# Kernel tuning notes

Hardware: AMD Instinct MI355X
Metric: run time of the kernel (lower is better)

The kernel has to match this reference:

```python
import jax, jax.numpy as jnp
import numpy as np
from jax import lax

# --- RPN config (eval / TEST path) ---
ASPECT = (0.5, 1.0, 2.0)
SCALE = (8.0, 16.0, 32.0)
STRIDE = 16
N_ANCHORS = len(ASPECT) * len(SCALE)  # 9
PRE_NMS = 6000
POST_NMS = 300
NMS_THRESH = 0.7
MIN_SIZE = 16.0
NEG = jnp.float32(-1e9)


def conv2d(x, w, b, pad):
    y = lax.conv_general_dilated(x, w, (1, 1), [(pad, pad), (pad, pad)],
                                 dimension_numbers=('NCHW', 'OIHW', 'NCHW'))
    return y + b[None, :, None, None]


def make_anchors(h, w):
    asp = jnp.array(ASPECT, jnp.float32)
    sc = jnp.array(SCALE, jnp.float32)
    size = float(STRIDE * STRIDE)
    ws = (jnp.sqrt(size / asp)[:, None] * sc[None, :]).reshape(-1)  # (A,)
    hs = (jnp.sqrt(size * asp)[:, None] * sc[None, :]).reshape(-1)
    c = (STRIDE - 1) / 2.0
    base = jnp.stack([c - 0.5 * (ws - 1), c - 0.5 * (hs - 1),
                      c + 0.5 * (ws - 1), c + 0.5 * (hs - 1)], axis=-1)  # (A,4)
    sx = jnp.arange(w, dtype=jnp.float32) * STRIDE
    sy = jnp.arange(h, dtype=jnp.float32) * STRIDE
    shift_x, shift_y = jnp.meshgrid(sx, sy)  # (h,w)
    shifts = jnp.stack([shift_x, shift_y, shift_x, shift_y], axis=-1)  # (h,w,4)
    return (shifts[:, :, None, :] + base[None, None]).reshape(-1, 4)  # (h*w*A,4)


def decode_boxes(anchors, deltas):
    wa = anchors[..., 2] - anchors[..., 0] + 1.0
    ha = anchors[..., 3] - anchors[..., 1] + 1.0
    cxa = anchors[..., 0] + 0.5 * wa
    cya = anchors[..., 1] + 0.5 * ha
    cx = deltas[..., 0] * wa + cxa
    cy = deltas[..., 1] * ha + cya
    pw = jnp.exp(deltas[..., 2]) * wa
    ph = jnp.exp(deltas[..., 3]) * ha
    return jnp.stack([cx - 0.5 * pw, cy - 0.5 * ph,
                      cx + 0.5 * pw, cy + 0.5 * ph], axis=-1)


def iou_one_many(box, boxes):
    x1 = jnp.maximum(box[0], boxes[:, 0])
    y1 = jnp.maximum(box[1], boxes[:, 1])
    x2 = jnp.minimum(box[2], boxes[:, 2])
    y2 = jnp.minimum(box[3], boxes[:, 3])
    inter = jnp.maximum(0.0, x2 - x1 + 1.0) * jnp.maximum(0.0, y2 - y1 + 1.0)
    a0 = (box[2] - box[0] + 1.0) * (box[3] - box[1] + 1.0)
    a1 = (boxes[:, 2] - boxes[:, 0] + 1.0) * (boxes[:, 3] - boxes[:, 1] + 1.0)
    return inter / (a0 + a1 - inter)


def nms_keep(boxes, scores):
    # boxes: (PRE,4) sorted by score desc; returns POST_NMS kept indices
    n = boxes.shape[0]

    def body(i, carry):
        valid, keep = carry
        s = jnp.where(valid, scores, NEG)
        j = jnp.argmax(s).astype(jnp.int32)
        keep = keep.at[i].set(j)
        iou = iou_one_many(boxes[j], boxes)
        valid = valid & (iou <= NMS_THRESH)
        valid = valid.at[j].set(False)
        return valid, keep

    _, keep = lax.fori_loop(0, POST_NMS, body,
                            (jnp.ones(n, bool), jnp.zeros(POST_NMS, jnp.int32)))
    return keep


def rpn_forward(input, im_info, w_feat, b_feat, w_cls, b_cls, w_reg, b_reg):
    feat = jax.nn.relu(conv2d(input, w_feat, b_feat, 1))  # (B,512,h,w)
    cls = conv2d(feat, w_cls, b_cls, 0)                    # (B,2A,h,w)
    B, _, h, w = cls.shape
    prob = jax.nn.softmax(cls.reshape(B, N_ANCHORS, 2, h, w), axis=2)
    fg = prob[:, :, 1]                                     # (B,A,h,w)
    scores = fg.transpose(0, 2, 3, 1).reshape(B, h * w * N_ANCHORS)
    reg = conv2d(feat, w_reg, b_reg, 0)                    # (B,4A,h,w)
    deltas = reg.transpose(0, 2, 3, 1).reshape(B, h * w * N_ANCHORS, 4)

    anchors = make_anchors(h, w)                           # (K,4)
    boxes = decode_boxes(anchors[None], deltas)            # (B,K,4)

    # clip to image
    im_h = im_info[:, 0][:, None]
    im_w = im_info[:, 1][:, None]
    x1 = jnp.clip(boxes[..., 0], 0.0, im_w - 1.0)
    y1 = jnp.clip(boxes[..., 1], 0.0, im_h - 1.0)
    x2 = jnp.clip(boxes[..., 2], 0.0, im_w - 1.0)
    y2 = jnp.clip(boxes[..., 3], 0.0, im_h - 1.0)
    boxes = jnp.stack([x1, y1, x2, y2], axis=-1)

    # min-size filter (mask scores instead of dropping rows)
    ms = MIN_SIZE * im_info[:, 2][:, None]
    ok = ((x2 - x1 + 1.0) >= ms) & ((y2 - y1 + 1.0) >= ms)
    scores = jnp.where(ok, scores, NEG)

    top_scores, order = lax.top_k(scores, PRE_NMS)         # (B,PRE)
    boxes_sorted = jnp.take_along_axis(boxes, order[..., None], axis=1)
    keep = jax.vmap(nms_keep)(boxes_sorted, top_scores)    # (B,POST)
    rois_boxes = jnp.take_along_axis(boxes_sorted, keep[..., None], axis=1)
    bidx = jnp.broadcast_to(jnp.arange(B, dtype=boxes.dtype)[:, None, None],
                            (B, POST_NMS, 1))
    return jnp.concatenate([bidx, rois_boxes], axis=-1)    # (B,POST,5)


def setup_inputs() -> dict:
    key = jax.random.key(0)
    ks = jax.random.split(key, 8)
    B, C, H, W = 8, 512, 64, 64
    inp = {
        'input': jax.random.normal(ks[0], (B, C, H, W), jnp.float32),
        'gt_box': jnp.zeros((B, 20, 5), jnp.float32),
        'im_info': jnp.tile(jnp.array([[1024.0, 1024.0, 1.0]], jnp.float32), (B, 1)),
        'w_feat': jax.random.normal(ks[1], (512, 512, 3, 3), jnp.float32) * 0.01,
        'b_feat': jnp.zeros((512,), jnp.float32),
        'w_cls': jax.random.normal(ks[2], (2 * N_ANCHORS, 512, 1, 1), jnp.float32) * 0.01,
        'b_cls': jnp.zeros((2 * N_ANCHORS,), jnp.float32),
        'w_reg': jax.random.normal(ks[3], (4 * N_ANCHORS, 512, 1, 1), jnp.float32) * 0.01,
        'b_reg': jnp.zeros((4 * N_ANCHORS,), jnp.float32),
    }
    return inp


def reference(input, gt_box, im_info, w_feat, b_feat, w_cls, b_cls, w_reg, b_reg):
    # eval-mode RPN: module returns (0, 0, rois); we return rois
    return rpn_forward(input, im_info, w_feat, b_feat, w_cls, b_cls, w_reg, b_reg)
```

## Files before the change

### kernel.cpp

```cpp
#include <hip/hip_runtime.h>
#include <hip/hip_bf16.h>
#include <stdint.h>

#define HW      64
#define CIN     512
#define KOUT    512
#define BATCH   8
#define NANCH   9
#define NBOX    (HW*HW*NANCH)
#define PRE_NMS 6000
#define POST_NMS 300
#define SORT_N  8192

__global__ __launch_bounds__(256, 2)
void conv3x3_relu(const float* __restrict__ in, const float* __restrict__ w,
                  const float* __restrict__ bias, float* __restrict__ feat) {
    __shared__ float s_in[2][8][6][68];
    __shared__ float s_w3[2][72 * 72];

    const int tid = threadIdx.x;
    const int k0  = blockIdx.x * 64;
    const int y0  = blockIdx.y * 4;
    const int b   = blockIdx.z;
    const int kg  = tid & 7;
    const int pos = tid >> 3;
    const int tx  = pos & 15;
    const int ty  = pos >> 4;
    const int x0  = tx * 4;

    int in_lds[3]; int in_goff[3]; bool in_ok[3];
#pragma unroll
    for (int s = 0; s < 3; ++s) {
        int v  = tid + 256 * s;
        int ci = v / 96, rem = v % 96;
        int r  = rem >> 4, c4 = rem & 15;
        int gy = y0 - 1 + r;
        in_ok[s]  = ((unsigned)gy < 64u);
        int gyc   = gy < 0 ? 0 : (gy > 63 ? 63 : gy);
        in_lds[s] = (ci * 6 + r) * 68 + 1 + 4 * c4;
        in_goff[s] = ((b * 512 + ci) * 64 + gyc) * 64 + 4 * c4;
    }
    int w_lds[5]; int w_goff[5]; bool w_ok[5];
#pragma unroll
    for (int s = 0; s < 5; ++s) {
        int q = tid + 256 * s;
        w_ok[s] = (q < 1152);
        int qq = w_ok[s] ? q : 0;
        int k = qq / 18, j4 = qq % 18;
        w_lds[s]  = (j4 * 4) * 72 + k;
        w_goff[s] = (k0 + k) * 4608 + 4 * j4;
    }

    for (int i = tid; i < 2 * 8 * 6 * 68; i += 256) ((float*)s_in)[i] = 0.0f;

    float4 pin[3], pw[5];
    auto prefetch = [&](int ch) {
#pragma unroll
        for (int s = 0; s < 3; ++s)
            pin[s] = *(const float4*)&in[in_goff[s] + ch * 4096];
#pragma unroll
        for (int s = 0; s < 5; ++s)
            pw[s] = *(const float4*)&w[w_goff[s] + ch * 9];
    };
    prefetch(0);

    float acc[2][8][4];
#pragma unroll
    for (int r = 0; r < 2; ++r)
#pragma unroll
        for (int k = 0; k < 8; ++k)
#pragma unroll
            for (int c = 0; c < 4; ++c) acc[r][k][c] = 0.0f;

    for (int cc8 = 0; cc8 < 64; ++cc8) {
        float* SIN = &s_in[cc8 & 1][0][0][0];
        float* SW  = &s_w3[cc8 & 1][0];

#pragma unroll
        for (int s = 0; s < 3; ++s) if (in_ok[s]) {
            SIN[in_lds[s] + 0] = pin[s].x;
            SIN[in_lds[s] + 1] = pin[s].y;
            SIN[in_lds[s] + 2] = pin[s].z;
            SIN[in_lds[s] + 3] = pin[s].w;
        }
#pragma unroll
        for (int s = 0; s < 5; ++s) if (w_ok[s]) {
            SW[w_lds[s] + 0 * 72] = pw[s].x;
            SW[w_lds[s] + 1 * 72] = pw[s].y;
            SW[w_lds[s] + 2 * 72] = pw[s].z;
            SW[w_lds[s] + 3 * 72] = pw[s].w;
        }
        __syncthreads();
        if (cc8 < 63) prefetch((cc8 + 1) * 8);

#pragma unroll
        for (int ci = 0; ci < 8; ++ci) {
#pragma unroll
            for (int dy = 0; dy < 3; ++dy) {
                float iv[2][6];
#pragma unroll
                for (int rr = 0; rr < 2; ++rr) {
                    int r = ty * 2 + rr + dy;
                    const float* rowp = &SIN[(ci * 6 + r) * 68];
                    float4 va = *(const float4*)&rowp[x0];
                    float2 vb = *(const float2*)&rowp[x0 + 4];
                    iv[rr][0] = va.x; iv[rr][1] = va.y; iv[rr][2] = va.z;
                    iv[rr][3] = va.w; iv[rr][4] = vb.x; iv[rr][5] = vb.y;
                }
#pragma unroll
                for (int dx = 0; dx < 3; ++dx) {
                    const float* wp = &SW[(ci * 9 + dy * 3 + dx) * 72 + kg * 8];
                    float4 w0v = *(const float4*)wp;
                    float4 w1v = *(const float4*)(wp + 4);
                    float wv[8] = {w0v.x, w0v.y, w0v.z, w0v.w,
                                   w1v.x, w1v.y, w1v.z, w1v.w};
#pragma unroll
                    for (int rr = 0; rr < 2; ++rr)
#pragma unroll
                        for (int k = 0; k < 8; ++k)
#pragma unroll
                            for (int c = 0; c < 4; ++c)
                                acc[rr][k][c] = fmaf(iv[rr][dx + c], wv[k], acc[rr][k][c]);
                }
            }
        }
    }
#pragma unroll
    for (int k = 0; k < 8; ++k) {
        float bv = bias[k0 + kg * 8 + k];
#pragma unroll
        for (int rr = 0; rr < 2; ++rr) {
            int y = y0 + ty * 2 + rr;
            float4 o;
            o.x = fmaxf(acc[rr][k][0] + bv, 0.0f);
            o.y = fmaxf(acc[rr][k][1] + bv, 0.0f);
            o.z = fmaxf(acc[rr][k][2] + bv, 0.0f);
            o.w = fmaxf(acc[rr][k][3] + bv, 0.0f);
            *(float4*)&feat[(((size_t)b * KOUT + k0 + kg * 8 + k) * HW + y) * HW + x0] = o;
        }
    }
}

__global__ __launch_bounds__(256, 2)
void heads(const float* __restrict__ feat,
           const float* __restrict__ wcls, const float* __restrict__ bcls,
           const float* __restrict__ wreg, const float* __restrict__ breg,
           const float* __restrict__ iminfo,
           unsigned long long* __restrict__ keys, float4* __restrict__ pbox) {
    __shared__ float s_w[128 * 56];

    const int tid = threadIdx.x;
    const int pix = blockIdx.x * 256 + tid;
    const int b   = pix >> 12;
    const int rem = pix & 4095;
    const int y   = rem >> 6;
    const int x   = rem & 63;

    float acc[54];
#pragma unroll
    for (int j = 0; j < 54; ++j) acc[j] = 0.0f;

    for (int cc = 0; cc < 512; cc += 128) {
        __syncthreads();
        for (int i = tid; i < 128 * 54; i += 256) {
            int j = i / 128; int cl = i % 128;
            float v = (j < 18) ? wcls[(size_t)j * 512 + cc + cl]
                               : wreg[(size_t)(j - 18) * 512 + cc + cl];
            s_w[cl * 56 + j] = v;
        }
        __syncthreads();
#pragma unroll 8
        for (int c2 = 0; c2 < 128; ++c2) {
            float f = feat[(((size_t)b * 512 + cc + c2) * 64 + y) * 64 + x];
#pragma unroll
            for (int j = 0; j < 54; ++j)
                acc[j] = fmaf(f, s_w[c2 * 56 + j], acc[j]);
        }
    }

    const float im_h = iminfo[b * 3 + 0];
    const float im_w = iminfo[b * 3 + 1];
    const float ms   = 16.0f * iminfo[b * 3 + 2];
    const float ASP[3] = {0.5f, 1.0f, 2.0f};
    const float SCL[3] = {8.0f, 16.0f, 32.0f};

#pragma unroll
    for (int a = 0; a < 9; ++a) {
        float c0 = acc[2 * a]     + bcls[2 * a];
        float c1 = acc[2 * a + 1] + bcls[2 * a + 1];
        float m  = fmaxf(c0, c1);
        float e0 = expf(c0 - m), e1 = expf(c1 - m);
        float fg = e1 / (e0 + e1);

        float d0 = acc[18 + 4 * a + 0] + breg[4 * a + 0];
        float d1 = acc[18 + 4 * a + 1] + breg[4 * a + 1];
        float d2 = acc[18 + 4 * a + 2] + breg[4 * a + 2];
        float d3 = acc[18 + 4 * a + 3] + breg[4 * a + 3];

        int ai = a / 3, si = a % 3;
        float wsz = sqrtf(256.0f / ASP[ai]) * SCL[si];
        float hsz = sqrtf(256.0f * ASP[ai]) * SCL[si];
        float sx = (float)x * 16.0f, sy = (float)y * 16.0f;
        float x1a = sx + (7.5f - 0.5f * (wsz - 1.0f));
        float y1a = sy + (7.5f - 0.5f * (hsz - 1.0f));
        float x2a = sx + (7.5f + 0.5f * (wsz - 1.0f));
        float y2a = sy + (7.5f + 0.5f * (hsz - 1.0f));

        float wa = x2a - x1a + 1.0f, ha = y2a - y1a + 1.0f;
        float cxa = x1a + 0.5f * wa, cya = y1a + 0.5f * ha;
        float cx = d0 * wa + cxa, cy = d1 * ha + cya;
        float pw = expf(d2) * wa, ph = expf(d3) * ha;
        float bx1 = cx - 0.5f * pw, by1 = cy - 0.5f * ph;
        float bx2 = cx + 0.5f * pw, by2 = cy + 0.5f * ph;

        bx1 = fminf(fmaxf(bx1, 0.0f), im_w - 1.0f);
        by1 = fminf(fmaxf(by1, 0.0f), im_h - 1.0f);
        bx2 = fminf(fmaxf(bx2, 0.0f), im_w - 1.0f);
        by2 = fminf(fmaxf(by2, 0.0f), im_h - 1.0f);

        bool ok = (bx2 - bx1 + 1.0f >= ms) && (by2 - by1 + 1.0f >= ms);
        float s = ok ? fg : -1e9f;

        unsigned u = __float_as_uint(s);
        u = (u & 0x80000000u) ? ~u : (u | 0x80000000u);
        int idx = (y * 64 + x) * 9 + a;
        keys[(size_t)b * NBOX + idx] =
            ((unsigned long long)u << 32) | (unsigned)(~(unsigned)idx);
        pbox[(size_t)b * NBOX + idx] = make_float4(bx1, by1, bx2, by2);
    }
}

__global__ __launch_bounds__(1024)
void select_sort(const unsigned long long* __restrict__ keys,
                 const float4* __restrict__ pbox,
                 float4* __restrict__ sorted) {
    __shared__ unsigned long long sbuf[SORT_N];
    __shared__ unsigned hist[16][256];
    __shared__ unsigned sh_prefix, sh_remaining, sh_counter;

    const int tid = threadIdx.x;
    const int b   = blockIdx.x;
    const int wv  = tid >> 6;
    const unsigned long long* kb = keys + (size_t)b * NBOX;

    if (tid == 0) { sh_prefix = 0u; sh_remaining = PRE_NMS; sh_counter = 0u; }

    for (int p = 3; p >= 0; --p) {
        for (int i = tid; i < 16 * 256; i += 1024) ((unsigned*)hist)[i] = 0u;
        __syncthreads();
        unsigned prefix = sh_prefix;
        unsigned pmask  = (p == 3) ? 0u : (0xFFFFFFFFu << (8 * (p + 1)));
        for (int i = tid; i < NBOX; i += 1024) {
            unsigned u = (unsigned)(kb[i] >> 32);
            if ((u & pmask) == prefix)
                atomicAdd(&hist[wv][(u >> (8 * p)) & 255], 1u);
        }
        __syncthreads();
        if (tid < 256) {
            unsigned s = 0;
#pragma unroll
            for (int w2 = 0; w2 < 16; ++w2) s += hist[w2][tid];
            hist[0][tid] = s;
        }
        __syncthreads();
        if (tid == 0) {
            unsigned rem = sh_remaining;
            int v = 255;
            for (; v > 0; --v) {
                unsigned c = hist[0][v];
                if (rem <= c) break;
                rem -= c;
            }
            sh_prefix    = prefix | ((unsigned)v << (8 * p));
            sh_remaining = rem;
        }
        __syncthreads();
    }
    const unsigned thr = sh_prefix;

    for (int i = tid; i < NBOX; i += 1024) {
        unsigned long long k = kb[i];
        bool act = ((unsigned)(k >> 32) >= thr);
        unsigned long long bal = __ballot(act);
        if (act) {
            int lane   = tid & 63;
            int leader = __ffsll(bal) - 1;
            unsigned base = 0;
            if (lane == leader) base = atomicAdd(&sh_counter, (unsigned)__popcll(bal));
            base = __shfl(base, leader);
            unsigned off = (unsigned)__popcll(bal & ((1ull << lane) - 1ull));
            unsigned pos2 = base + off;
            if (pos2 < SORT_N) sbuf[pos2] = k;
        }
    }
    __syncthreads();
    unsigned n = sh_counter; if (n > SORT_N) n = SORT_N;
    for (int i = (int)n + tid; i < SORT_N; i += 1024) sbuf[i] = 0ull;
    __syncthreads();

    for (int k = 2; k <= SORT_N; k <<= 1) {
        for (int j = k >> 1; j > 0; j >>= 1) {
            for (int t = tid; t < SORT_N / 2; t += 1024) {
                int i  = ((t & ~(j - 1)) << 1) | (t & (j - 1));
                int ix = i | j;
                bool up = ((i & k) == 0);
                unsigned long long a = sbuf[i], c = sbuf[ix];
                bool sw = up ? (a < c) : (a > c);
                if (sw) { sbuf[i] = c; sbuf[ix] = a; }
            }
            __syncthreads();
        }
    }

    for (int i = tid; i < PRE_NMS; i += 1024) {
        unsigned idx = ~((unsigned)sbuf[i]);
        sorted[(size_t)b * PRE_NMS + i] = pbox[(size_t)b * NBOX + idx];
    }
}

__global__ __launch_bounds__(512, 2)
void nms(const float4* __restrict__ sorted, float* __restrict__ out) {
    __shared__ unsigned long long vmask[94];
    __shared__ int sh_j;

    const int tid = threadIdx.x;
    const int b   = blockIdx.x;
    const float4* sb = sorted + (size_t)b * PRE_NMS;

    float4 bx[12]; float ar[12];
#pragma unroll
    for (int s = 0; s < 12; ++s) {
        int i = tid + 512 * s;
        if (i < PRE_NMS) {
            float4 v = sb[i];
            bx[s] = v;
            ar[s] = (v.z - v.x + 1.0f) * (v.w - v.y + 1.0f);
        } else {
            bx[s] = make_float4(0.f, 0.f, 0.f, 0.f);
            ar[s] = 1.0f;
        }
    }
    if (tid < 94) vmask[tid] = (tid < 93) ? ~0ull : ((1ull << 48) - 1ull);
    __syncthreads();

    for (int it = 0; it < POST_NMS; ++it) {
        if (tid < 64) {
            unsigned long long w0 = vmask[tid];
            unsigned long long w1 = (tid < 30) ? vmask[tid + 64] : 0ull;
            int cand = w0 ? (tid * 64 + __ffsll(w0) - 1)
                          : (w1 ? ((tid + 64) * 64 + __ffsll(w1) - 1) : 0x7FFFFFFF);
#pragma unroll
            for (int off = 32; off > 0; off >>= 1) {
                int o = __shfl_xor(cand, off);
                cand = (o < cand) ? o : cand;
            }
            if (tid == 0) sh_j = (cand == 0x7FFFFFFF) ? 0 : cand;
        }
        __syncthreads();
        int j = sh_j;
        float4 jb = sb[j];
        if (tid == 0) {
            float* o = out + ((size_t)b * POST_NMS + it) * 5;
            o[0] = (float)b; o[1] = jb.x; o[2] = jb.y; o[3] = jb.z; o[4] = jb.w;
        }
        float ja = (jb.z - jb.x + 1.0f) * (jb.w - jb.y + 1.0f);
#pragma unroll
        for (int s = 0; s < 12; ++s) {
            int i = tid + 512 * s;
            if (i < PRE_NMS && ((vmask[i >> 6] >> (i & 63)) & 1ull)) {
                float xx1 = fmaxf(jb.x, bx[s].x);
                float yy1 = fmaxf(jb.y, bx[s].y);
                float xx2 = fminf(jb.z, bx[s].z);
                float yy2 = fminf(jb.w, bx[s].w);
                float inter = fmaxf(0.0f, xx2 - xx1 + 1.0f) *
                              fmaxf(0.0f, yy2 - yy1 + 1.0f);
                float iou = inter / (ja + ar[s] - inter);
                if (iou > 0.7f)
                    atomicAnd(&vmask[i >> 6], ~(1ull << (i & 63)));
            }
        }
        __syncthreads();
    }
}

extern "C" void kernel_launch(void* const* d_in, const int* in_sizes, int n_in,
                              void* d_out, int out_size, void* d_ws, size_t ws_size,
                              hipStream_t stream) {
    (void)in_sizes; (void)n_in; (void)out_size; (void)ws_size;
    const float* input  = (const float*)d_in[0];
    const float* iminfo = (const float*)d_in[2];
    const float* wfeat  = (const float*)d_in[3];
    const float* bfeat  = (const float*)d_in[4];
    const float* wcls   = (const float*)d_in[5];
    const float* bcls   = (const float*)d_in[6];
    const float* wreg   = (const float*)d_in[7];
    const float* breg   = (const float*)d_in[8];
    float* out = (float*)d_out;

    char* ws = (char*)d_ws;
    float*               feat   = (float*)ws;
    unsigned long long*  keys   = (unsigned long long*)(ws + 67108864);
    float4*              pbox   = (float4*)(ws + 67108864 + 2359296);
    float4*              sorted = (float4*)(ws + 67108864 + 2359296 + 4718592);

    conv3x3_relu<<<dim3(8, 16, 8), 256, 0, stream>>>(input, wfeat, bfeat, feat);
    heads<<<dim3(128), 256, 0, stream>>>(feat, wcls, bcls, wreg, breg, iminfo, keys, pbox);
    select_sort<<<dim3(8), 1024, 0, stream>>>(keys, pbox, sorted);
    nms<<<dim3(8), 512, 0, stream>>>(sorted, out);
}
```

Baseline: 3.177 ms.

## Pre-transpose conv weights and double conv tile height with unpadded input tiles

Adds a kernel that transposes the 3x3 conv weights to [cin*9][kout] once per call, so weight tiles load as coalesced float4 rows and store to LDS as float4 instead of scattered scalars. The conv tile grows from 4 to 8 output rows per block, giving 4 rows x 8 channels x 4 columns of accumulators per thread. This raises FMA reuse of each weight load and halves the grid. Input rows are stored unpadded and the x-halo is read per element with edge masking. The cost is higher register pressure under launch_bounds(256,2), an extra launch, and reuse of the keys workspace region for the transposed weights, which heads later overwrites.

```diff
diff --git a/kernel.cpp b/kernel.cpp
--- a/kernel.cpp
+++ b/kernel.cpp
@@ -12,15 +12,33 @@
 #define POST_NMS 300
 #define SORT_N  8192
 
+__global__ __launch_bounds__(256)
+void transpose_w(const float* __restrict__ w, float* __restrict__ wt) {
+    __shared__ float t[32][33];
+    const int jt = blockIdx.x * 32, kt = blockIdx.y * 32;
+    const int c  = threadIdx.x & 31, r8 = threadIdx.x >> 5;
+#pragma unroll
+    for (int p = 0; p < 4; ++p) {
+        int kl = r8 + p * 8;
+        t[kl][c] = w[(size_t)(kt + kl) * 4608 + jt + c];
+    }
+    __syncthreads();
+#pragma unroll
+    for (int p = 0; p < 4; ++p) {
+        int jl = r8 + p * 8;
+        wt[(size_t)(jt + jl) * 512 + kt + c] = t[c][jl];
+    }
+}
+
 __global__ __launch_bounds__(256, 2)
-void conv3x3_relu(const float* __restrict__ in, const float* __restrict__ w,
+void conv3x3_relu(const float* __restrict__ in, const float* __restrict__ wt,
                   const float* __restrict__ bias, float* __restrict__ feat) {
-    __shared__ float s_in[2][8][6][68];
-    __shared__ float s_w3[2][72 * 72];
+    __shared__ float s_in[2][8][10][64];
+    __shared__ float s_w[2][72][64];
 
     const int tid = threadIdx.x;
     const int k0  = blockIdx.x * 64;
-    const int y0  = blockIdx.y * 4;
+    const int y0  = blockIdx.y * 8;
     const int b   = blockIdx.z;
     const int kg  = tid & 7;
     const int pos = tid >> 3;
@@ -28,16 +46,16 @@
     const int ty  = pos >> 4;
     const int x0  = tx * 4;
 
-    int in_lds[3]; int in_goff[3]; bool in_ok[3];
-#pragma unroll
-    for (int s = 0; s < 3; ++s) {
-        int v  = tid + 256 * s;
-        int ci = v / 96, rem = v % 96;
+    int in_lds[5]; int in_goff[5]; bool in_ok[5];
+#pragma unroll
+    for (int s = 0; s < 5; ++s) {
+        int q  = tid + 256 * s;
+        int ci = q / 160, rem = q % 160;
         int r  = rem >> 4, c4 = rem & 15;
         int gy = y0 - 1 + r;
         in_ok[s]  = ((unsigned)gy < 64u);
         int gyc   = gy < 0 ? 0 : (gy > 63 ? 63 : gy);
-        in_lds[s] = (ci * 6 + r) * 68 + 1 + 4 * c4;
+        in_lds[s] = (ci * 10 + r) * 64 + 4 * c4;
         in_goff[s] = ((b * 512 + ci) * 64 + gyc) * 64 + 4 * c4;
     }
     int w_lds[5]; int w_goff[5]; bool w_ok[5];
@@ -46,27 +64,26 @@
         int q = tid + 256 * s;
         w_ok[s] = (q < 1152);
         int qq = w_ok[s] ? q : 0;
-        int k = qq / 18, j4 = qq % 18;
-        w_lds[s]  = (j4 * 4) * 72 + k;
-        w_goff[s] = (k0 + k) * 4608 + 4 * j4;
-    }
-
-    for (int i = tid; i < 2 * 8 * 6 * 68; i += 256) ((float*)s_in)[i] = 0.0f;
-
-    float4 pin[3], pw[5];
-    auto prefetch = [&](int ch) {
-#pragma unroll
-        for (int s = 0; s < 3; ++s)
-            pin[s] = *(const float4*)&in[in_goff[s] + ch * 4096];
+        int jl = qq / 16, k4 = qq % 16;
+        w_lds[s]  = jl * 64 + 4 * k4;
+        w_goff[s] = jl * 512 + k0 + 4 * k4;
+    }
+
+    float4 pin[5], pw[5];
+    const float4 z4 = make_float4(0.f, 0.f, 0.f, 0.f);
+    auto prefetch = [&](int cc8) {
 #pragma unroll
         for (int s = 0; s < 5; ++s)
-            pw[s] = *(const float4*)&w[w_goff[s] + ch * 9];
+            pin[s] = in_ok[s] ? *(const float4*)&in[in_goff[s] + cc8 * 32768] : z4;
+#pragma unroll
+        for (int s = 0; s < 5; ++s)
+            if (w_ok[s]) pw[s] = *(const float4*)&wt[(size_t)cc8 * 36864 + w_goff[s]];
     };
     prefetch(0);
 
-    float acc[2][8][4];
-#pragma unroll
-    for (int r = 0; r < 2; ++r)
+    float acc[4][8][4];
+#pragma unroll
+    for (int r = 0; r < 4; ++r)
 #pragma unroll
         for (int k = 0; k < 8; ++k)
 #pragma unroll
@@ -74,53 +91,49 @@
 
     for (int cc8 = 0; cc8 < 64; ++cc8) {
         float* SIN = &s_in[cc8 & 1][0][0][0];
-        float* SW  = &s_w3[cc8 & 1][0];
-
-#pragma unroll
-        for (int s = 0; s < 3; ++s) if (in_ok[s]) {
-            SIN[in_lds[s] + 0] = pin[s].x;
-            SIN[in_lds[s] + 1] = pin[s].y;
-            SIN[in_lds[s] + 2] = pin[s].z;
-            SIN[in_lds[s] + 3] = pin[s].w;
-        }
-#pragma unroll
-        for (int s = 0; s < 5; ++s) if (w_ok[s]) {
-            SW[w_lds[s] + 0 * 72] = pw[s].x;
-            SW[w_lds[s] + 1 * 72] = pw[s].y;
-            SW[w_lds[s] + 2 * 72] = pw[s].z;
-            SW[w_lds[s] + 3 * 72] = pw[s].w;
-        }
-        __syncthreads();
-        if (cc8 < 63) prefetch((cc8 + 1) * 8);
+        float* SW  = &s_w[cc8 & 1][0][0];
+
+#pragma unroll
+        for (int s = 0; s < 5; ++s)
+            *(float4*)&SIN[in_lds[s]] = pin[s];
+#pragma unroll
+        for (int s = 0; s < 5; ++s)
+            if (w_ok[s]) *(float4*)&SW[w_lds[s]] = pw[s];
+        __syncthreads();
+        if (cc8 < 63) prefetch(cc8 + 1);
 
 #pragma unroll
         for (int ci = 0; ci < 8; ++ci) {
 #pragma unroll
             for (int dy = 0; dy < 3; ++dy) {
-                float iv[2][6];
-#pragma unroll
-                for (int rr = 0; rr < 2; ++rr) {
-                    int r = ty * 2 + rr + dy;
-                    const float* rowp = &SIN[(ci * 6 + r) * 68];
-                    float4 va = *(const float4*)&rowp[x0];
-                    float2 vb = *(const float2*)&rowp[x0 + 4];
-                    iv[rr][0] = va.x; iv[rr][1] = va.y; iv[rr][2] = va.z;
-                    iv[rr][3] = va.w; iv[rr][4] = vb.x; iv[rr][5] = vb.y;
+                float jv[4][6];
+#pragma unroll
+                for (int rr = 0; rr < 4; ++rr) {
+                    int rw = ty * 4 + rr + dy;
+                    const float* rp = &SIN[(ci * 10 + rw) * 64];
+                    float4 va = *(const float4*)&rp[x0];
+                    int al = (tx > 0) ? (x0 - 1) : 0;
+                    int ar = (tx < 15) ? (x0 + 4) : 0;
+                    float lv = rp[al], rv = rp[ar];
+                    jv[rr][0] = (tx > 0) ? lv : 0.0f;
+                    jv[rr][1] = va.x; jv[rr][2] = va.y;
+                    jv[rr][3] = va.z; jv[rr][4] = va.w;
+                    jv[rr][5] = (tx < 15) ? rv : 0.0f;
                 }
 #pragma unroll
                 for (int dx = 0; dx < 3; ++dx) {
-                    const float* wp = &SW[(ci * 9 + dy * 3 + dx) * 72 + kg * 8];
+                    const float* wp = &SW[(ci * 9 + dy * 3 + dx) * 64 + kg * 8];
                     float4 w0v = *(const float4*)wp;
                     float4 w1v = *(const float4*)(wp + 4);
                     float wv[8] = {w0v.x, w0v.y, w0v.z, w0v.w,
                                    w1v.x, w1v.y, w1v.z, w1v.w};
 #pragma unroll
-                    for (int rr = 0; rr < 2; ++rr)
+                    for (int rr = 0; rr < 4; ++rr)
 #pragma unroll
                         for (int k = 0; k < 8; ++k)
 #pragma unroll
                             for (int c = 0; c < 4; ++c)
-                                acc[rr][k][c] = fmaf(iv[rr][dx + c], wv[k], acc[rr][k][c]);
+                                acc[rr][k][c] = fmaf(jv[rr][dx + c], wv[k], acc[rr][k][c]);
                 }
             }
         }
@@ -129,8 +142,8 @@
     for (int k = 0; k < 8; ++k) {
         float bv = bias[k0 + kg * 8 + k];
 #pragma unroll
-        for (int rr = 0; rr < 2; ++rr) {
-            int y = y0 + ty * 2 + rr;
+        for (int rr = 0; rr < 4; ++rr) {
+            int y = y0 + ty * 4 + rr;
             float4 o;
             o.x = fmaxf(acc[rr][k][0] + bv, 0.0f);
             o.y = fmaxf(acc[rr][k][1] + bv, 0.0f);
@@ -399,11 +412,13 @@
 
     char* ws = (char*)d_ws;
     float*               feat   = (float*)ws;
+    float*               wt     = (float*)(ws + 67108864);
     unsigned long long*  keys   = (unsigned long long*)(ws + 67108864);
     float4*              pbox   = (float4*)(ws + 67108864 + 2359296);
     float4*              sorted = (float4*)(ws + 67108864 + 2359296 + 4718592);
 
-    conv3x3_relu<<<dim3(8, 16, 8), 256, 0, stream>>>(input, wfeat, bfeat, feat);
+    transpose_w<<<dim3(144, 16), 256, 0, stream>>>(wfeat, wt);
+    conv3x3_relu<<<dim3(8, 8, 8), 256, 0, stream>>>(input, wt, bfeat, feat);
     heads<<<dim3(128), 256, 0, stream>>>(feat, wcls, bcls, wreg, breg, iminfo, keys, pbox);
     select_sort<<<dim3(8), 1024, 0, stream>>>(keys, pbox, sorted);
     nms<<<dim3(8), 512, 0, stream>>>(sorted, out);
```

After: 3.517 ms. 1.11x slower.
